# Optimization experiments

Measured on AMD Instinct MI355X. Metric: run time of the kernel, lower is better.

The kernel has to match this reference:

```python
import jax, jax.numpy as jnp
import numpy as np

D_MODEL = 1024
NUM_HEADS = 16
HEAD_DIM = D_MODEL // NUM_HEADS


def setup_inputs() -> dict:
    key = jax.random.key(0)
    k1, k2, k3, k4, k5 = jax.random.split(key, 5)
    B, S = 2, 2048
    X = jax.random.normal(k1, (B, S, D_MODEL), dtype=jnp.float32)
    Wqkv = jax.random.normal(k2, (3 * D_MODEL, D_MODEL), dtype=jnp.float32) * 0.02
    bqkv = jax.random.normal(k3, (3 * D_MODEL,), dtype=jnp.float32) * 0.02
    Wo = jax.random.normal(k4, (D_MODEL, D_MODEL), dtype=jnp.float32) * 0.02
    bo = jax.random.normal(k5, (D_MODEL,), dtype=jnp.float32) * 0.02
    return {"X": X, "Wqkv": Wqkv, "bqkv": bqkv, "Wo": Wo, "bo": bo}


def reference(X, Wqkv, bqkv, Wo, bo):
    B, S, D = X.shape
    # fused QKV projection (torch Linear: x @ W.T + b)
    qkv = X @ Wqkv.T + bqkv                                  # [B, S, 3D]
    qkv = qkv.reshape(B, S, NUM_HEADS, 3 * HEAD_DIM)
    qkv = jnp.transpose(qkv, (0, 2, 1, 3))                   # [B, H, S, 3*hd]
    q, k, v = jnp.split(qkv, 3, axis=-1)                     # each [B, H, S, hd]
    # naive scaled dot-product attention (materializes full SxS scores)
    scale = 1.0 / jnp.sqrt(jnp.asarray(HEAD_DIM, dtype=X.dtype))
    scores = jnp.einsum("bhqd,bhkd->bhqk", q, k) * scale     # [B, H, S, S]
    attn = jax.nn.softmax(scores, axis=-1)
    values = jnp.einsum("bhqk,bhkd->bhqd", attn, v)          # [B, H, S, hd]
    values = jnp.transpose(values, (0, 2, 1, 3)).reshape(B, S, D)
    return values @ Wo.T + bo
```

## Files before the change

kernel.cpp:

```cpp
#include <hip/hip_runtime.h>

#define DM    1024
#define NH    16
#define HD    64
#define SEQ   2048
#define BATCH 2
#define NQKV  3072
#define MTOT  4096

using half2v = __attribute__((ext_vector_type(2))) _Float16;
using half4  = __attribute__((ext_vector_type(4))) _Float16;
using half8  = __attribute__((ext_vector_type(8))) _Float16;
using f32x4  = __attribute__((ext_vector_type(4))) float;

typedef const __attribute__((address_space(1))) unsigned int* gp_t;
typedef __attribute__((address_space(3))) unsigned int* lp_t;

__device__ __forceinline__ void gl2lds16(const void* g, void* l) {
    __builtin_amdgcn_global_load_lds((gp_t)g, (lp_t)l, 16, 0, 0);
}

__device__ __forceinline__ f32x4 fzero4() {
    f32x4 v; v[0] = 0.f; v[1] = 0.f; v[2] = 0.f; v[3] = 0.f; return v;
}

__device__ __forceinline__ int sw8(int row, int col) {
    return (row << 6) | ((((col >> 3) ^ row) & 7) << 3) | (col & 7);
}

#define CSCALE 0.18033688011112042f

__device__ __forceinline__ half2v expp2(float a, float b) {
    return __builtin_bit_cast(half2v, __builtin_amdgcn_cvt_pkrtz(
        __builtin_amdgcn_exp2f(a), __builtin_amdgcn_exp2f(b)));
}

__global__ __launch_bounds__(256) void cvt_all(const float* __restrict__ X,
                                               const float* __restrict__ W1,
                                               const float* __restrict__ W2,
                                               const float* __restrict__ bqkv,
                                               float* __restrict__ bscaled,
                                               _Float16* __restrict__ out) {
    const int nX = MTOT * DM / 4, nW1 = NQKV * DM / 4, nW2 = DM * DM / 4;
    int i = blockIdx.x * 256 + threadIdx.x;
    if (i < NQKV) {
        const float b = bqkv[i];
        bscaled[i] = ((i % 192) < 64) ? b * CSCALE : b;
    }
    if (i >= nX + nW1 + nW2) return;
    float4 f;
    float sc = 1.0f;
    if (i < nX) {
        f = reinterpret_cast<const float4*>(X)[i];
    } else if (i < nX + nW1) {
        const int off = i - nX;
        f = reinterpret_cast<const float4*>(W1)[off];
        const int row = off >> 8;
        if ((row % 192) < 64) sc = CSCALE;
    } else {
        f = reinterpret_cast<const float4*>(W2)[i - nX - nW1];
    }
    half4 h;
    h[0] = (_Float16)(f.x * sc); h[1] = (_Float16)(f.y * sc);
    h[2] = (_Float16)(f.z * sc); h[3] = (_Float16)(f.w * sc);
    reinterpret_cast<half4*>(out)[i] = h;
}

template <bool OUT_F16>
__global__ __launch_bounds__(256) void gemm_nt(const _Float16* __restrict__ A,
                                               const _Float16* __restrict__ B,
                                               const float* __restrict__ bias,
                                               void* __restrict__ Cout,
                                               int M, int N, int K) {
    __shared__ _Float16 lA[128 * 64];
    __shared__ _Float16 lB[128 * 64];
    const int tid = threadIdx.x;
    const int m0 = blockIdx.y * 128, n0 = blockIdx.x * 128;
    const int wave = tid >> 6, lane = tid & 63, quad = lane >> 4, l15 = lane & 15;
    const int wm = (wave & 1) * 64, wn = (wave >> 1) * 64;

    f32x4 acc[4][4];
#pragma unroll
    for (int i = 0; i < 4; ++i)
#pragma unroll
        for (int j = 0; j < 4; ++j) acc[i][j] = fzero4();

    const int cperm = (((tid & 7) ^ (tid >> 3)) & 7) * 8;
    const _Float16* Ab = A + (long)(m0 + (tid >> 3)) * K + cperm;
    const _Float16* Bb = B + (long)(n0 + (tid >> 3)) * K + cperm;
    char* lAp = (char*)lA + tid * 16;
    char* lBp = (char*)lB + tid * 16;

    for (int kt = 0; kt < K; kt += 64) {
        __syncthreads();
#pragma unroll
        for (int j = 0; j < 4; ++j) {
            gl2lds16(Ab + (long)j * 32 * K + kt, lAp + j * 4096);
            gl2lds16(Bb + (long)j * 32 * K + kt, lBp + j * 4096);
        }
        __syncthreads();
#pragma unroll
        for (int ks = 0; ks < 2; ++ks) {
            half8 af[4], bfr[4];
#pragma unroll
            for (int t = 0; t < 4; ++t) {
                af[t]  = *(const half8*)(lA + sw8(wm + t * 16 + l15, ks * 32 + quad * 8));
                bfr[t] = *(const half8*)(lB + sw8(wn + t * 16 + l15, ks * 32 + quad * 8));
            }
#pragma unroll
            for (int mt = 0; mt < 4; ++mt)
#pragma unroll
                for (int nt = 0; nt < 4; ++nt)
                    acc[mt][nt] = __builtin_amdgcn_mfma_f32_16x16x32_f16(
                        af[mt], bfr[nt], acc[mt][nt], 0, 0, 0);
        }
    }

    float bs[4];
#pragma unroll
    for (int nt = 0; nt < 4; ++nt) bs[nt] = bias[n0 + wn + nt * 16 + l15];

#pragma unroll
    for (int mt = 0; mt < 4; ++mt) {
#pragma unroll
        for (int r = 0; r < 4; ++r) {
            const int m = m0 + wm + mt * 16 + quad * 4 + r;
#pragma unroll
            for (int nt = 0; nt < 4; ++nt) {
                const int n = n0 + wn + nt * 16 + l15;
                const float v = acc[mt][nt][r] + bs[nt];
                if constexpr (OUT_F16)
                    ((_Float16*)Cout)[(long)m * N + n] = (_Float16)v;
                else
                    ((float*)Cout)[(long)m * N + n] = v;
            }
        }
    }
}

template <bool OUT_F16>
__global__ __launch_bounds__(256) void gemm_nt_64(const _Float16* __restrict__ A,
                                                  const _Float16* __restrict__ B,
                                                  const float* __restrict__ bias,
                                                  void* __restrict__ Cout,
                                                  int M, int N, int K) {
    __shared__ _Float16 lA[64 * 64];
    __shared__ _Float16 lB[128 * 64];
    const int tid = threadIdx.x;
    const int m0 = blockIdx.y * 64, n0 = blockIdx.x * 128;
    const int wave = tid >> 6, lane = tid & 63, quad = lane >> 4, l15 = lane & 15;
    const int wm = (wave & 1) * 32, wn = (wave >> 1) * 64;

    f32x4 acc[2][4];
#pragma unroll
    for (int i = 0; i < 2; ++i)
#pragma unroll
        for (int j = 0; j < 4; ++j) acc[i][j] = fzero4();

    const int cperm = (((tid & 7) ^ (tid >> 3)) & 7) * 8;
    const _Float16* Ab = A + (long)(m0 + (tid >> 3)) * K + cperm;
    const _Float16* Bb = B + (long)(n0 + (tid >> 3)) * K + cperm;
    char* lAp = (char*)lA + tid * 16;
    char* lBp = (char*)lB + tid * 16;

    for (int kt = 0; kt < K; kt += 64) {
        __syncthreads();
#pragma unroll
        for (int j = 0; j < 2; ++j)
            gl2lds16(Ab + (long)j * 32 * K + kt, lAp + j * 4096);
#pragma unroll
        for (int j = 0; j < 4; ++j)
            gl2lds16(Bb + (long)j * 32 * K + kt, lBp + j * 4096);
        __syncthreads();
#pragma unroll
        for (int ks = 0; ks < 2; ++ks) {
            half8 af[2], bfr[4];
#pragma unroll
            for (int t = 0; t < 2; ++t)
                af[t] = *(const half8*)(lA + sw8(wm + t * 16 + l15, ks * 32 + quad * 8));
#pragma unroll
            for (int t = 0; t < 4; ++t)
                bfr[t] = *(const half8*)(lB + sw8(wn + t * 16 + l15, ks * 32 + quad * 8));
#pragma unroll
            for (int mt = 0; mt < 2; ++mt)
#pragma unroll
                for (int nt = 0; nt < 4; ++nt)
                    acc[mt][nt] = __builtin_amdgcn_mfma_f32_16x16x32_f16(
                        af[mt], bfr[nt], acc[mt][nt], 0, 0, 0);
        }
    }

    float bs[4];
#pragma unroll
    for (int nt = 0; nt < 4; ++nt) bs[nt] = bias[n0 + wn + nt * 16 + l15];

#pragma unroll
    for (int mt = 0; mt < 2; ++mt) {
#pragma unroll
        for (int r = 0; r < 4; ++r) {
            const int m = m0 + wm + mt * 16 + quad * 4 + r;
#pragma unroll
            for (int nt = 0; nt < 4; ++nt) {
                const int n = n0 + wn + nt * 16 + l15;
                const float v = acc[mt][nt][r] + bs[nt];
                if constexpr (OUT_F16)
                    ((_Float16*)Cout)[(long)m * N + n] = (_Float16)v;
                else
                    ((float*)Cout)[(long)m * N + n] = v;
            }
        }
    }
}

__global__ __launch_bounds__(256) void repack_v(const _Float16* __restrict__ qkvh,
                                                _Float16* __restrict__ vt) {
    const int b = blockIdx.z, h = blockIdx.y, s0 = blockIdx.x * 32;
    const int d = threadIdx.x & 63, si = threadIdx.x >> 6;
    const _Float16* src = qkvh + (long)(b * SEQ + s0) * NQKV + h * 192 + 128 + d;
    half8 v;
#pragma unroll
    for (int hi = 0; hi < 2; ++hi)
#pragma unroll
        for (int r = 0; r < 4; ++r)
            v[hi * 4 + r] = src[(long)(hi * 16 + si * 4 + r) * NQKV];
    *(half8*)(vt + (long)((b * NH + h) * HD + d) * SEQ + s0 + si * 8) = v;
}

__global__ __launch_bounds__(256) void attn_flash(const _Float16* __restrict__ qkv,
                                                  const _Float16* __restrict__ vt,
                                                  _Float16* __restrict__ aout) {
    __shared__ _Float16 lKV[4][64 * 64];

    const int L = blockIdx.x + 32 * blockIdx.y + 512 * blockIdx.z;
    const int c = L & 7, j = L >> 3;
    const int pair = c * 4 + (j >> 5);
    const int b = pair >> 4, h = pair & 15;
    const int q0 = (j & 31) * 64;

    const int tid = threadIdx.x;
    const int wave = tid >> 6, lane = tid & 63, quad = lane >> 4, l15 = lane & 15;
    const int cperm8 = (((tid & 7) ^ (tid >> 3)) & 7) * 8;

    const _Float16* qsrc = qkv + (long)(b * SEQ + q0 + (tid >> 3)) * NQKV + h * 192 + cperm8;
#pragma unroll
    for (int jq = 0; jq < 2; ++jq)
        gl2lds16(qsrc + (long)jq * 32 * NQKV, (char*)lKV + jq * 4096 + tid * 16);
    __syncthreads();

    half8 qf[2];
#pragma unroll
    for (int ks = 0; ks < 2; ++ks)
        qf[ks] = *(const half8*)(lKV[0] + sw8(wave * 16 + l15, ks * 32 + quad * 8));
    __syncthreads();

    f32x4 O[4];
#pragma unroll
    for (int dt = 0; dt < 4; ++dt) O[dt] = fzero4();
    f32x4 lsum = fzero4();

    half8 ones;
#pragma unroll
    for (int i = 0; i < 8; ++i) ones[i] = (_Float16)1.0f;

    const _Float16* ksrc = qkv + (long)(b * SEQ + (tid >> 3)) * NQKV + h * 192 + 64 + cperm8;
    const _Float16* vsrc = vt + (long)((b * NH + h) * HD + (tid >> 3)) * SEQ + cperm8;

#pragma unroll
    for (int jj = 0; jj < 2; ++jj) {
        gl2lds16(ksrc + (long)(jj * 32) * NQKV, (char*)lKV[0] + jj * 4096 + tid * 16);
        gl2lds16(vsrc + (long)(jj * 32) * SEQ,  (char*)lKV[2] + jj * 4096 + tid * 16);
    }
    __syncthreads();

    for (int it = 0; it < 32; ++it) {
        const int cur = it & 1;
        if (it < 31) {
            const int s0n = (it + 1) * 64;
#pragma unroll
            for (int jj = 0; jj < 2; ++jj) {
                gl2lds16(ksrc + (long)(s0n + jj * 32) * NQKV, (char*)lKV[cur ^ 1] + jj * 4096 + tid * 16);
                gl2lds16(vsrc + (long)(jj * 32) * SEQ + s0n,  (char*)lKV[2 + (cur ^ 1)] + jj * 4096 + tid * 16);
            }
        }
        const _Float16* lK = lKV[cur];
        const _Float16* lV = lKV[2 + cur];

#pragma unroll
        for (int t = 0; t < 2; ++t) {
            f32x4 s[2];
            s[0] = fzero4(); s[1] = fzero4();
#pragma unroll
            for (int tt = 0; tt < 2; ++tt) {
#pragma unroll
                for (int ks = 0; ks < 2; ++ks) {
                    half8 kf = *(const half8*)(lK + sw8((2 * t + tt) * 16 + l15, ks * 32 + quad * 8));
                    s[tt] = __builtin_amdgcn_mfma_f32_16x16x32_f16(kf, qf[ks], s[tt], 0, 0, 0);
                }
            }
            half2v p01 = expp2(s[0][0], s[0][1]);
            half2v p23 = expp2(s[0][2], s[0][3]);
            half2v p45 = expp2(s[1][0], s[1][1]);
            half2v p67 = expp2(s[1][2], s[1][3]);
            half4 lo = __builtin_shufflevector(p01, p23, 0, 1, 2, 3);
            half4 hi = __builtin_shufflevector(p45, p67, 0, 1, 2, 3);
            half8 pf = __builtin_shufflevector(lo, hi, 0, 1, 2, 3, 4, 5, 6, 7);
            lsum = __builtin_amdgcn_mfma_f32_16x16x32_f16(pf, ones, lsum, 0, 0, 0);
#pragma unroll
            for (int dt = 0; dt < 4; ++dt) {
                half8 vf = *(const half8*)(lV + sw8(dt * 16 + l15, t * 32 + quad * 8));
                O[dt] = __builtin_amdgcn_mfma_f32_16x16x32_f16(pf, vf, O[dt], 0, 0, 0);
            }
        }
        __syncthreads();
    }

#pragma unroll
    for (int r = 0; r < 4; ++r) {
        const float lr = 1.0f / lsum[r];
        const int row = b * SEQ + q0 + wave * 16 + quad * 4 + r;
#pragma unroll
        for (int dt = 0; dt < 4; ++dt)
            aout[(long)row * DM + h * HD + dt * 16 + l15] =
                (_Float16)(O[dt][r] * lr);
    }
}

extern "C" void kernel_launch(void* const* d_in, const int* in_sizes, int n_in,
                              void* d_out, int out_size, void* d_ws, size_t ws_size,
                              hipStream_t stream) {
    const float* X    = (const float*)d_in[0];
    const float* Wqkv = (const float*)d_in[1];
    const float* bqkv = (const float*)d_in[2];
    const float* Wo   = (const float*)d_in[3];
    const float* bo   = (const float*)d_in[4];

    char* ws = (char*)d_ws;
    _Float16* Xh   = (_Float16*)(ws);
    _Float16* Wqh  = (_Float16*)(ws + (size_t)8  * 1048576);
    _Float16* Woh  = (_Float16*)(ws + (size_t)14 * 1048576);
    _Float16* qkvh = (_Float16*)(ws + (size_t)16 * 1048576);
    _Float16* vth  = (_Float16*)(ws + (size_t)40 * 1048576);
    _Float16* atth = (_Float16*)(ws + (size_t)48 * 1048576);
    float* bscaled = (float*)(ws + (size_t)48 * 1048576);

    const int ncvt = (MTOT * DM + NQKV * DM + DM * DM) / 4;
    cvt_all<<<(ncvt + 255) / 256, 256, 0, stream>>>(X, Wqkv, Wo, bqkv, bscaled, Xh);

    gemm_nt<true><<<dim3(NQKV / 128, MTOT / 128), 256, 0, stream>>>(
        Xh, Wqh, bscaled, qkvh, MTOT, NQKV, DM);

    repack_v<<<dim3(SEQ / 32, NH, BATCH), 256, 0, stream>>>(qkvh, vth);

    attn_flash<<<dim3(SEQ / 64, NH, BATCH), 256, 0, stream>>>(qkvh, vth, atth);

    gemm_nt_64<false><<<dim3(DM / 128, MTOT / 64), 256, 0, stream>>>(
        atth, Woh, bo, d_out, MTOT, DM, DM);
}
```

Baseline: 195.7 us.

## Triple-buffer K/V tiles with 512-thread attention blocks and explicit vmcnt barriers

The flash attention kernel now uses 512-thread blocks covering 128 query rows, so each K/V tile loaded into LDS is shared by eight waves instead of four. The double buffer becomes a three-stage ring, prefetching two tiles ahead, and waits use explicit s_waitcnt vmcnt plus raw barriers in place of __syncthreads. The aim is to halve K/V global traffic per query row and keep loads further ahead of the MFMA work. The cost is more LDS per block (48KB) and fewer blocks in the grid, which may reduce occupancy.

```diff
diff --git a/kernel.cpp b/kernel.cpp
--- a/kernel.cpp
+++ b/kernel.cpp
@@ -34,6 +34,19 @@
     return __builtin_bit_cast(half2v, __builtin_amdgcn_cvt_pkrtz(
         __builtin_amdgcn_exp2f(a), __builtin_amdgcn_exp2f(b)));
 }
+
+#define ACQ(N) do {                                             \
+    asm volatile("s_waitcnt vmcnt(" #N ")" ::: "memory");       \
+    __builtin_amdgcn_sched_barrier(0);                          \
+    __builtin_amdgcn_s_barrier();                               \
+    __builtin_amdgcn_sched_barrier(0);                          \
+} while (0)
+#define REL() do {                                              \
+    __builtin_amdgcn_sched_barrier(0);                          \
+    asm volatile("s_waitcnt lgkmcnt(0)" ::: "memory");          \
+    __builtin_amdgcn_s_barrier();                               \
+    __builtin_amdgcn_sched_barrier(0);                          \
+} while (0)
 
 __global__ __launch_bounds__(256) void cvt_all(const float* __restrict__ X,
                                                const float* __restrict__ W1,
@@ -226,31 +239,31 @@
     *(half8*)(vt + (long)((b * NH + h) * HD + d) * SEQ + s0 + si * 8) = v;
 }
 
-__global__ __launch_bounds__(256) void attn_flash(const _Float16* __restrict__ qkv,
+__global__ __launch_bounds__(512) void attn_flash(const _Float16* __restrict__ qkv,
                                                   const _Float16* __restrict__ vt,
                                                   _Float16* __restrict__ aout) {
-    __shared__ _Float16 lKV[4][64 * 64];
-
-    const int L = blockIdx.x + 32 * blockIdx.y + 512 * blockIdx.z;
+    __shared__ _Float16 lbuf[6][64 * 64];
+
+    const int L = blockIdx.x + 16 * blockIdx.y + 256 * blockIdx.z;
     const int c = L & 7, j = L >> 3;
-    const int pair = c * 4 + (j >> 5);
+    const int pair = c * 4 + (j >> 4);
     const int b = pair >> 4, h = pair & 15;
-    const int q0 = (j & 31) * 64;
+    const int q0 = (j & 15) * 128;
 
     const int tid = threadIdx.x;
     const int wave = tid >> 6, lane = tid & 63, quad = lane >> 4, l15 = lane & 15;
     const int cperm8 = (((tid & 7) ^ (tid >> 3)) & 7) * 8;
-
-    const _Float16* qsrc = qkv + (long)(b * SEQ + q0 + (tid >> 3)) * NQKV + h * 192 + cperm8;
-#pragma unroll
-    for (int jq = 0; jq < 2; ++jq)
-        gl2lds16(qsrc + (long)jq * 32 * NQKV, (char*)lKV + jq * 4096 + tid * 16);
+    const int srow = tid >> 3;
+
+    const _Float16* qsrc = qkv + (long)(b * SEQ + q0 + srow) * NQKV + h * 192 + cperm8;
+    gl2lds16(qsrc,                    (char*)lbuf + tid * 16);
+    gl2lds16(qsrc + (long)64 * NQKV,  (char*)lbuf + 8192 + tid * 16);
     __syncthreads();
 
     half8 qf[2];
 #pragma unroll
     for (int ks = 0; ks < 2; ++ks)
-        qf[ks] = *(const half8*)(lKV[0] + sw8(wave * 16 + l15, ks * 32 + quad * 8));
+        qf[ks] = *(const half8*)((const _Float16*)lbuf + sw8(wave * 16 + l15, ks * 32 + quad * 8));
     __syncthreads();
 
     f32x4 O[4];
@@ -262,41 +275,26 @@
 #pragma unroll
     for (int i = 0; i < 8; ++i) ones[i] = (_Float16)1.0f;
 
-    const _Float16* ksrc = qkv + (long)(b * SEQ + (tid >> 3)) * NQKV + h * 192 + 64 + cperm8;
-    const _Float16* vsrc = vt + (long)((b * NH + h) * HD + (tid >> 3)) * SEQ + cperm8;
-
-#pragma unroll
-    for (int jj = 0; jj < 2; ++jj) {
-        gl2lds16(ksrc + (long)(jj * 32) * NQKV, (char*)lKV[0] + jj * 4096 + tid * 16);
-        gl2lds16(vsrc + (long)(jj * 32) * SEQ,  (char*)lKV[2] + jj * 4096 + tid * 16);
-    }
-    __syncthreads();
-
-    for (int it = 0; it < 32; ++it) {
-        const int cur = it & 1;
-        if (it < 31) {
-            const int s0n = (it + 1) * 64;
-#pragma unroll
-            for (int jj = 0; jj < 2; ++jj) {
-                gl2lds16(ksrc + (long)(s0n + jj * 32) * NQKV, (char*)lKV[cur ^ 1] + jj * 4096 + tid * 16);
-                gl2lds16(vsrc + (long)(jj * 32) * SEQ + s0n,  (char*)lKV[2 + (cur ^ 1)] + jj * 4096 + tid * 16);
-            }
-        }
-        const _Float16* lK = lKV[cur];
-        const _Float16* lV = lKV[2 + cur];
-
+    const _Float16* ksrc = qkv + (long)(b * SEQ + srow) * NQKV + h * 192 + 64 + cperm8;
+    const _Float16* vsrc = vt + (long)((b * NH + h) * HD + srow) * SEQ + cperm8;
+
+    gl2lds16(ksrc,                   (char*)lbuf[0] + tid * 16);
+    gl2lds16(vsrc,                   (char*)lbuf[3] + tid * 16);
+    gl2lds16(ksrc + (long)64 * NQKV, (char*)lbuf[1] + tid * 16);
+    gl2lds16(vsrc + 64,              (char*)lbuf[4] + tid * 16);
+
+    auto compute = [&](const _Float16* lK, const _Float16* lV) {
 #pragma unroll
         for (int t = 0; t < 2; ++t) {
             f32x4 s[2];
             s[0] = fzero4(); s[1] = fzero4();
 #pragma unroll
-            for (int tt = 0; tt < 2; ++tt) {
+            for (int tt = 0; tt < 2; ++tt)
 #pragma unroll
                 for (int ks = 0; ks < 2; ++ks) {
                     half8 kf = *(const half8*)(lK + sw8((2 * t + tt) * 16 + l15, ks * 32 + quad * 8));
                     s[tt] = __builtin_amdgcn_mfma_f32_16x16x32_f16(kf, qf[ks], s[tt], 0, 0, 0);
                 }
-            }
             half2v p01 = expp2(s[0][0], s[0][1]);
             half2v p23 = expp2(s[0][2], s[0][3]);
             half2v p45 = expp2(s[1][0], s[1][1]);
@@ -311,8 +309,25 @@
                 O[dt] = __builtin_amdgcn_mfma_f32_16x16x32_f16(pf, vf, O[dt], 0, 0, 0);
             }
         }
-        __syncthreads();
-    }
+    };
+
+    int cur = 0;
+    for (int it = 0; it < 30; ++it) {
+        int pre = cur + 2; if (pre >= 3) pre -= 3;
+        const long s0n = (long)(it + 2) * 64;
+        gl2lds16(ksrc + s0n * NQKV, (char*)lbuf[pre] + tid * 16);
+        gl2lds16(vsrc + s0n,        (char*)lbuf[3 + pre] + tid * 16);
+        ACQ(4);
+        compute(lbuf[cur], lbuf[3 + cur]);
+        REL();
+        cur = (cur == 2) ? 0 : cur + 1;
+    }
+    ACQ(2);
+    compute(lbuf[cur], lbuf[3 + cur]);
+    REL();
+    cur = (cur == 2) ? 0 : cur + 1;
+    ACQ(0);
+    compute(lbuf[cur], lbuf[3 + cur]);
 
 #pragma unroll
     for (int r = 0; r < 4; ++r) {
@@ -351,7 +366,7 @@
 
     repack_v<<<dim3(SEQ / 32, NH, BATCH), 256, 0, stream>>>(qkvh, vth);
 
-    attn_flash<<<dim3(SEQ / 64, NH, BATCH), 256, 0, stream>>>(qkvh, vth, atth);
+    attn_flash<<<dim3(SEQ / 128, NH, BATCH), 512, 0, stream>>>(qkvh, vth, atth);
 
     gemm_nt_64<false><<<dim3(DM / 128, MTOT / 64), 256, 0, stream>>>(
         atth, Woh, bo, d_out, MTOT, DM, DM);
```

After: 183.7 us. 6.2% less time.
